# Kernel optimization log

Hardware: AMD Instinct MI355X
Metric: run time of the kernel (lower is better)

The kernel has to match this reference:

```python
import jax, jax.numpy as jnp
import numpy as np

THETA = 1.0
V_TH = 1.0       # spikingjelly IFNode default v_threshold
SG_ALPHA = 4.0   # spikingjelly surrogate.Sigmoid default alpha


@jax.custom_vjp
def heaviside(x):
    # spike = 1 if membrane - threshold >= 0
    return (x >= 0).astype(x.dtype)

def _heaviside_fwd(x):
    return (x >= 0).astype(x.dtype), x

def _heaviside_bwd(x, g):
    s = jax.nn.sigmoid(SG_ALPHA * x)
    return (g * SG_ALPHA * s * (1.0 - s),)

heaviside.defvjp(_heaviside_fwd, _heaviside_bwd)


@jax.custom_vjp
def spike_aggregate(spike_out, z_total):
    return spike_out

def _sa_fwd(spike_out, z_total):
    return spike_out, z_total

def _sa_bwd(z_total, g):
    surrogate = (z_total > 0).astype(g.dtype) / THETA
    return (jnp.zeros_like(g), g * surrogate)

spike_aggregate.defvjp(_sa_fwd, _sa_bwd)


def setup_inputs() -> dict:
    key = jax.random.key(0)
    k_x, k_w1, k_b1, k_w2, k_b2 = jax.random.split(key, 5)
    B, D_in, H, D_out = 4096, 784, 800, 10
    x = jax.random.uniform(k_x, (B, D_in), dtype=jnp.float32)
    # nn.Linear-style init: U(-1/sqrt(fan_in), 1/sqrt(fan_in))
    s1 = 1.0 / np.sqrt(D_in)
    s2 = 1.0 / np.sqrt(H)
    W1 = jax.random.uniform(k_w1, (H, D_in), jnp.float32, -s1, s1)
    b1 = jax.random.uniform(k_b1, (H,), jnp.float32, -s1, s1)
    W2 = jax.random.uniform(k_w2, (D_out, H), jnp.float32, -s2, s2)
    b2 = jax.random.uniform(k_b2, (D_out,), jnp.float32, -s2, s2)
    return {"x": x, "W1": W1, "b1": b1, "W2": W2, "b2": b2, "T_sim": 32}


def reference(x, W1, b1, W2, b2, T_sim):
    B = x.shape[0]
    x = x.reshape(B, -1)
    # fixed Bernoulli rate encoding (rand_like(x) < x)
    u = jax.random.uniform(jax.random.key(42), x.shape, dtype=x.dtype)
    x_fixed = (u < x).astype(x.dtype)
    # fc1 input is the same every timestep -> compute once
    cur1 = x_fixed @ W1.T + b1                     # [B, 800]

    def step(carry, _):
        v1, v2, count, z_total = carry
        h1 = v1 + cur1
        spk1 = heaviside(h1 - V_TH)
        v1 = h1 * (1.0 - jax.lax.stop_gradient(spk1))  # hard reset to 0, detach_reset
        cur2 = spk1 @ W2.T + b2                    # [B, 10]
        z_total = z_total + cur2
        h2 = v2 + cur2
        spk2 = heaviside(h2 - V_TH)
        v2 = h2 * (1.0 - jax.lax.stop_gradient(spk2))
        count = count + spk2
        return (v1, v2, count, z_total), None

    H, D_out = W1.shape[0], W2.shape[0]
    init = (jnp.zeros((B, H), x.dtype), jnp.zeros((B, D_out), x.dtype),
            jnp.zeros((B, D_out), x.dtype), jnp.zeros((B, D_out), x.dtype))
    (v1, v2, count, z_total), _ = jax.lax.scan(step, init, None, length=T_sim)
    return spike_aggregate(count, z_total)
```

## Files before the change

### kernel.cpp

```cpp
#include <hip/hip_runtime.h>
#include <stdint.h>

#define B_ROWS 4096
#define D_IN   784
#define H_DIM  800
#define D_OUT  10
#define T_SIM  32
#define N_ELEM (B_ROWS * D_IN)
#define CAP    448
#define R_PER  2

__device__ __forceinline__ void threefry2x32(uint32_t k0, uint32_t k1,
                                             uint32_t& x0, uint32_t& x1) {
  uint32_t ks0 = k0, ks1 = k1, ks2 = k0 ^ k1 ^ 0x1BD11BDAu;
  x0 += ks0; x1 += ks1;
#define TF_RND(r) { x0 += x1; x1 = (x1 << (r)) | (x1 >> (32 - (r))); x1 ^= x0; }
  TF_RND(13) TF_RND(15) TF_RND(26) TF_RND(6)
  x0 += ks1; x1 += ks2 + 1u;
  TF_RND(17) TF_RND(29) TF_RND(16) TF_RND(24)
  x0 += ks2; x1 += ks0 + 2u;
  TF_RND(13) TF_RND(15) TF_RND(26) TF_RND(6)
  x0 += ks0; x1 += ks1 + 3u;
  TF_RND(17) TF_RND(29) TF_RND(16) TF_RND(24)
  x0 += ks1; x1 += ks2 + 4u;
  TF_RND(13) TF_RND(15) TF_RND(26) TF_RND(6)
  x0 += ks2; x1 += ks0 + 5u;
#undef TF_RND
}

__global__ __launch_bounds__(256) void gen_xfixed(const float* __restrict__ x,
                                                  float* __restrict__ xf) {
  int i = blockIdx.x * blockDim.x + threadIdx.x;
  if (i >= N_ELEM) return;
  uint32_t c0 = 0u, c1 = (uint32_t)i;
  threefry2x32(0u, 42u, c0, c1);
  uint32_t bits = c0 ^ c1;
  float u = __uint_as_float((bits >> 9) | 0x3F800000u) - 1.0f;
  xf[i] = (u < x[i]) ? 1.0f : 0.0f;
}

#define BM 128
#define BN 64
#define BK 16

__global__ __launch_bounds__(256) void gemm_periods(const float* __restrict__ xf,
                                                    const float* __restrict__ W1,
                                                    const float* __restrict__ b1,
                                                    uint8_t* __restrict__ pb) {
  __shared__ __align__(16) float As[BK][BM + 4];
  __shared__ __align__(16) float Bs[BK][BN + 4];
  const int m0 = blockIdx.y * BM;
  const int n0 = blockIdx.x * BN;
  const int t  = threadIdx.x;
  const int tx = t & 15, ty = t >> 4;
  const int ar = t >> 1;
  const int ak = (t & 1) * 8;
  const int br = t >> 2;
  const int bk = (t & 3) * 4;
  const int hB = n0 + br;
  const bool bOK = (hB < H_DIM);
  const float* aptr = xf + (m0 + ar) * D_IN + ak;
  const float* bptr = W1 + (bOK ? hB : 0) * D_IN + bk;

  float4 a0 = *(const float4*)(aptr);
  float4 a1 = *(const float4*)(aptr + 4);
  float4 b0 = *(const float4*)(bptr);
  if (!bOK) { b0.x = b0.y = b0.z = b0.w = 0.0f; }

  float acc[8][4] = {};
  for (int kt = 0; kt < D_IN; kt += BK) {
    As[ak + 0][ar] = a0.x; As[ak + 1][ar] = a0.y;
    As[ak + 2][ar] = a0.z; As[ak + 3][ar] = a0.w;
    As[ak + 4][ar] = a1.x; As[ak + 5][ar] = a1.y;
    As[ak + 6][ar] = a1.z; As[ak + 7][ar] = a1.w;
    Bs[bk + 0][br] = b0.x; Bs[bk + 1][br] = b0.y;
    Bs[bk + 2][br] = b0.z; Bs[bk + 3][br] = b0.w;
    __syncthreads();
    if (kt + BK < D_IN) {
      a0 = *(const float4*)(aptr + kt + BK);
      a1 = *(const float4*)(aptr + kt + BK + 4);
      b0 = *(const float4*)(bptr + kt + BK);
      if (!bOK) { b0.x = b0.y = b0.z = b0.w = 0.0f; }
    }
#pragma unroll
    for (int kk = 0; kk < BK; kk++) {
      float4 av0 = *(const float4*)&As[kk][ty * 8];
      float4 av1 = *(const float4*)&As[kk][ty * 8 + 4];
      float4 bv  = *(const float4*)&Bs[kk][tx * 4];
      float a[8] = {av0.x, av0.y, av0.z, av0.w, av1.x, av1.y, av1.z, av1.w};
      float b[4] = {bv.x, bv.y, bv.z, bv.w};
#pragma unroll
      for (int mi = 0; mi < 8; mi++)
#pragma unroll
        for (int ni = 0; ni < 4; ni++)
          acc[mi][ni] = __builtin_fmaf(a[mi], b[ni], acc[mi][ni]);
    }
    __syncthreads();
  }
  const int hOut = n0 + tx * 4;
  if (hOut < H_DIM) {
    float4 bb = *(const float4*)&b1[hOut];
#pragma unroll
    for (int mi = 0; mi < 8; mi++) {
      int m = m0 + ty * 8 + mi;
      float c4[4];
      c4[0] = acc[mi][0] + bb.x;
      c4[1] = acc[mi][1] + bb.y;
      c4[2] = acc[mi][2] + bb.z;
      c4[3] = acc[mi][3] + bb.w;
      uint32_t packed = 0;
#pragma unroll
      for (int ni = 0; ni < 4; ni++) {
        float c = c4[ni];
        float v = 0.0f;
        int p = 0;
#pragma unroll 1
        for (int s = 1; s <= T_SIM; s++) {
          float h1 = v + c;
          if (h1 >= 1.0f) { p = s; break; }
          v = h1;
        }
        packed |= (uint32_t)p << (8 * ni);
      }
      *(uint32_t*)&pb[(size_t)m * H_DIM + hOut] = packed;
    }
  }
}

__global__ __launch_bounds__(320) void snn_scan(const uint8_t* __restrict__ pb,
                                                const float* __restrict__ W2,
                                                const float* __restrict__ b2,
                                                float* __restrict__ out) {
  __shared__ __align__(16) float W2T[H_DIM * D_OUT];
  __shared__ uint16_t ha16[R_PER][CAP];
  __shared__ uint32_t mks[R_PER][CAP];
  __shared__ int      lenL[R_PER];
  __shared__ uint32_t mask_tbl[T_SIM + 1];
  __shared__ float    c2s[R_PER][T_SIM][D_OUT];
  __shared__ float    b2f[D_OUT];
  const int tid  = threadIdx.x;
  const int row0 = blockIdx.x * R_PER;

  if (tid < D_OUT) b2f[tid] = b2[tid];
  if (tid <= T_SIM) {
    uint32_t mk = 0;
    if (tid > 0) for (int s = tid; s <= T_SIM; s += tid) mk |= 1u << (s - 1);
    mask_tbl[tid] = mk;
  }
  __syncthreads();

  if (tid < 128) {
    const int r = tid >> 6, ln = tid & 63;
    const uint64_t lmask = (1ull << ln) - 1ull;
    uint8_t pv[13];
#pragma unroll
    for (int ch = 0; ch < 13; ch++) {
      int h = ch * 64 + ln;
      pv[ch] = (h < H_DIM) ? pb[(size_t)(row0 + r) * H_DIM + h] : (uint8_t)0;
    }
    int off = 0;
#pragma unroll
    for (int ch = 0; ch < 13; ch++) {
      int h = ch * 64 + ln;
      int p = pv[ch];
      bool g = (p != 0);
      uint64_t bal = __ballot(g);
      int pos = off + __popcll(bal & lmask);
      if (g && pos < CAP) {
        ha16[r][pos] = (uint16_t)(h * 40);
        mks[r][pos]  = mask_tbl[p];
      }
      off += __popcll(bal);
    }
    if (ln == 0) lenL[r] = off;
  } else {
    for (int e = tid - 128; e < H_DIM * D_OUT; e += 192) {
      int o = e / H_DIM, h = e - o * H_DIM;
      W2T[h * D_OUT + o] = W2[e];
    }
  }
  __syncthreads();

  const int L0 = min(lenL[0], CAP), L1 = min(lenL[1], CAP);
  for (int e = tid; e < R_PER * CAP; e += 320) {
    int r = e / CAP, i = e - r * CAP;
    if (i >= (r ? L1 : L0)) { mks[r][i] = 0u; ha16[r][i] = 0; }
  }
  __syncthreads();

  {
    const int t = tid & 31, r = (tid >> 5) & 1, j = tid >> 6;
    float s0 = 0.0f, s1 = 0.0f;
    if (lenL[0] <= CAP && lenL[1] <= CAP) {
      const int Lmax = max(L0, L1);
      const uint16_t* hp = ha16[r];
      const uint32_t* mp = mks[r];
      const float*    wbase = W2T + 2 * j;
#pragma unroll 8
      for (int i = 0; i < Lmax; i++) {
        uint32_t ha = hp[i];
        uint32_t mk = mp[i];
        float2 w = *(const float2*)((const char*)wbase + ha);
        bool g = (mk >> t) & 1u;
        s0 += g ? w.x : 0.0f;
        s1 += g ? w.y : 0.0f;
      }
    } else {
      const uint8_t* prow = pb + (size_t)(row0 + r) * H_DIM;
      for (int h = 0; h < H_DIM; h++) {
        uint32_t mk = mask_tbl[prow[h]];
        float2 w = *(const float2*)&W2T[h * D_OUT + 2 * j];
        bool g = (mk >> t) & 1u;
        s0 += g ? w.x : 0.0f;
        s1 += g ? w.y : 0.0f;
      }
    }
    c2s[r][t][2 * j]     = s0;
    c2s[r][t][2 * j + 1] = s1;
  }
  __syncthreads();

  if (tid < R_PER * D_OUT) {
    const int r = tid / D_OUT, o = tid % D_OUT;
    const float bb = b2f[o];
    float v = 0.0f; int cnt = 0;
#pragma unroll
    for (int t = 0; t < T_SIM; t++) {
      float cur2 = c2s[r][t][o] + bb;
      float h2 = v + cur2;
      bool spk = (h2 >= 1.0f);
      cnt += spk ? 1 : 0;
      v = spk ? 0.0f : h2;
    }
    out[(size_t)(row0 + r) * D_OUT + o] = (float)cnt;
  }
}

extern "C" void kernel_launch(void* const* d_in, const int* in_sizes, int n_in,
                              void* d_out, int out_size, void* d_ws, size_t ws_size,
                              hipStream_t stream) {
  const float* x  = (const float*)d_in[0];
  const float* W1 = (const float*)d_in[1];
  const float* b1 = (const float*)d_in[2];
  const float* W2 = (const float*)d_in[3];
  const float* b2 = (const float*)d_in[4];
  float* outp = (float*)d_out;

  float*   xf = (float*)d_ws;
  uint8_t* pbuf = (uint8_t*)(xf + N_ELEM);

  gen_xfixed<<<N_ELEM / 256, 256, 0, stream>>>(x, xf);

  dim3 g1((H_DIM + BN - 1) / BN, B_ROWS / BM);
  gemm_periods<<<g1, 256, 0, stream>>>(xf, W1, b1, pbuf);

  snn_scan<<<B_ROWS / R_PER, 320, 0, stream>>>(pbuf, W2, b2, outp);
}
```

Before: 296.8 us.

## Gather W2 columns per active neuron into staged smem and widen scan block

```diff
diff --git a/kernel.cpp b/kernel.cpp
--- a/kernel.cpp
+++ b/kernel.cpp
@@ -7,8 +7,7 @@
 #define D_OUT  10
 #define T_SIM  32
 #define N_ELEM (B_ROWS * D_IN)
-#define CAP    448
-#define R_PER  2
+#define CAP    512
 
 __device__ __forceinline__ void threefry2x32(uint32_t k0, uint32_t k1,
                                              uint32_t& x0, uint32_t& x1) {
@@ -103,11 +102,8 @@
 #pragma unroll
     for (int mi = 0; mi < 8; mi++) {
       int m = m0 + ty * 8 + mi;
-      float c4[4];
-      c4[0] = acc[mi][0] + bb.x;
-      c4[1] = acc[mi][1] + bb.y;
-      c4[2] = acc[mi][2] + bb.z;
-      c4[3] = acc[mi][3] + bb.w;
+      float c4[4] = {acc[mi][0] + bb.x, acc[mi][1] + bb.y,
+                     acc[mi][2] + bb.z, acc[mi][3] + bb.w};
       uint32_t packed = 0;
 #pragma unroll
       for (int ni = 0; ni < 4; ni++) {
@@ -127,105 +123,122 @@
   }
 }
 
-__global__ __launch_bounds__(320) void snn_scan(const uint8_t* __restrict__ pb,
+__global__ __launch_bounds__(640) void snn_scan(const uint8_t* __restrict__ pb,
                                                 const float* __restrict__ W2,
                                                 const float* __restrict__ b2,
                                                 float* __restrict__ out) {
-  __shared__ __align__(16) float W2T[H_DIM * D_OUT];
-  __shared__ uint16_t ha16[R_PER][CAP];
-  __shared__ uint32_t mks[R_PER][CAP];
-  __shared__ int      lenL[R_PER];
-  __shared__ uint32_t mask_tbl[T_SIM + 1];
-  __shared__ float    c2s[R_PER][T_SIM][D_OUT];
+  __shared__ __align__(8) uint32_t mkS[2][CAP];
+  __shared__ uint16_t hidxS[2][CAP];
+  __shared__ __align__(16) float wst[2 * 5 * (CAP / 2) * 4];
+  __shared__ int      lenS[2];
+  __shared__ uint32_t mtbl[T_SIM + 1];
+  __shared__ float    c2s[2][T_SIM][D_OUT];
   __shared__ float    b2f[D_OUT];
   const int tid  = threadIdx.x;
-  const int row0 = blockIdx.x * R_PER;
-
-  if (tid < D_OUT) b2f[tid] = b2[tid];
+  const int row0 = blockIdx.x * 2;
+
   if (tid <= T_SIM) {
     uint32_t mk = 0;
-    if (tid > 0) for (int s = tid; s <= T_SIM; s += tid) mk |= 1u << (s - 1);
-    mask_tbl[tid] = mk;
-  }
+    if (tid) for (int s = tid; s <= T_SIM; s += tid) mk |= 1u << (s - 1);
+    mtbl[tid] = mk;
+  }
+  if (tid < D_OUT) b2f[tid] = b2[tid];
   __syncthreads();
 
   if (tid < 128) {
     const int r = tid >> 6, ln = tid & 63;
-    const uint64_t lmask = (1ull << ln) - 1ull;
+    const uint64_t lm = (1ull << ln) - 1ull;
+    const uint8_t* prow = pb + (size_t)(row0 + r) * H_DIM;
     uint8_t pv[13];
 #pragma unroll
-    for (int ch = 0; ch < 13; ch++) {
+    for (int ch = 0; ch < 13; ++ch) {
       int h = ch * 64 + ln;
-      pv[ch] = (h < H_DIM) ? pb[(size_t)(row0 + r) * H_DIM + h] : (uint8_t)0;
+      pv[ch] = (h < H_DIM) ? prow[h] : (uint8_t)0;
     }
     int off = 0;
 #pragma unroll
-    for (int ch = 0; ch < 13; ch++) {
-      int h = ch * 64 + ln;
-      int p = pv[ch];
-      bool g = (p != 0);
+    for (int ch = 0; ch < 13; ++ch) {
+      bool g = (pv[ch] != 0);
       uint64_t bal = __ballot(g);
-      int pos = off + __popcll(bal & lmask);
+      int pos = off + __popcll(bal & lm);
       if (g && pos < CAP) {
-        ha16[r][pos] = (uint16_t)(h * 40);
-        mks[r][pos]  = mask_tbl[p];
+        hidxS[r][pos] = (uint16_t)(ch * 64 + ln);
+        mkS[r][pos]   = mtbl[pv[ch]];
       }
       off += __popcll(bal);
     }
-    if (ln == 0) lenL[r] = off;
-  } else {
-    for (int e = tid - 128; e < H_DIM * D_OUT; e += 192) {
-      int o = e / H_DIM, h = e - o * H_DIM;
-      W2T[h * D_OUT + o] = W2[e];
-    }
-  }
-  __syncthreads();
-
-  const int L0 = min(lenL[0], CAP), L1 = min(lenL[1], CAP);
-  for (int e = tid; e < R_PER * CAP; e += 320) {
-    int r = e / CAP, i = e - r * CAP;
-    if (i >= (r ? L1 : L0)) { mks[r][i] = 0u; ha16[r][i] = 0; }
+    if (ln == 0) lenS[r] = off;
+  }
+  __syncthreads();
+
+  const int L0 = min(lenS[0], CAP), L1 = min(lenS[1], CAP);
+  const bool ovf = (lenS[0] > CAP) || (lenS[1] > CAP);
+  const int Lpad = (max(L0, L1) + 63) & ~63;
+
+  for (int e = tid; e < 2 * CAP; e += 640) {
+    int r = e >= CAP ? 1 : 0, i = e - r * CAP;
+    if (i >= (r ? L1 : L0)) mkS[r][i] = 0u;
   }
   __syncthreads();
 
   {
-    const int t = tid & 31, r = (tid >> 5) & 1, j = tid >> 6;
-    float s0 = 0.0f, s1 = 0.0f;
-    if (lenL[0] <= CAP && lenL[1] <= CAP) {
-      const int Lmax = max(L0, L1);
-      const uint16_t* hp = ha16[r];
-      const uint32_t* mp = mks[r];
-      const float*    wbase = W2T + 2 * j;
-#pragma unroll 8
-      for (int i = 0; i < Lmax; i++) {
-        uint32_t ha = hp[i];
-        uint32_t mk = mp[i];
-        float2 w = *(const float2*)((const char*)wbase + ha);
-        bool g = (mk >> t) & 1u;
-        s0 += g ? w.x : 0.0f;
-        s1 += g ? w.y : 0.0f;
+    const int npairs = Lpad >> 1;
+    for (int e = tid; e < 10 * npairs * 2; e += 640) {
+      int tmpe = e;
+      int hi = tmpe & 1; tmpe >>= 1;
+      int i2 = tmpe % npairs; tmpe /= npairs;
+      int j = tmpe % 5;  int r = tmpe / 5;
+      const int o = 2 * j + hi;
+      const int Lr = r ? L1 : L0;
+      float2 w;
+      int i0 = 2 * i2;
+      w.x = (i0     < Lr) ? W2[o * H_DIM + hidxS[r][i0]]     : 0.0f;
+      w.y = (i0 + 1 < Lr) ? W2[o * H_DIM + hidxS[r][i0 + 1]] : 0.0f;
+      *(float2*)&wst[((r * 5 + j) * (CAP / 2) + i2) * 4 + hi * 2] = w;
+    }
+  }
+  __syncthreads();
+
+  {
+    const int wv = tid >> 6;
+    const int r = wv & 1, j = wv >> 1;
+    const int lane = tid & 63;
+    const int t = lane & 31;
+    const int hi = lane >> 5;
+    float s = 0.0f;
+    if (!ovf) {
+      const uint32_t* mbase = mkS[r];
+      const float* wbase = &wst[(r * 5 + j) * (CAP / 2) * 4 + hi * 2];
+      const int npairs = Lpad >> 1;
+#pragma unroll 4
+      for (int i2 = 0; i2 < npairs; ++i2) {
+        uint2 mk2 = *(const uint2*)&mbase[2 * i2];
+        float2 w2 = *(const float2*)(wbase + i2 * 4);
+        float g0 = (float)((mk2.x >> t) & 1u);
+        s = __builtin_fmaf(g0, w2.x, s);
+        float g1 = (float)((mk2.y >> t) & 1u);
+        s = __builtin_fmaf(g1, w2.y, s);
       }
     } else {
       const uint8_t* prow = pb + (size_t)(row0 + r) * H_DIM;
-      for (int h = 0; h < H_DIM; h++) {
-        uint32_t mk = mask_tbl[prow[h]];
-        float2 w = *(const float2*)&W2T[h * D_OUT + 2 * j];
-        bool g = (mk >> t) & 1u;
-        s0 += g ? w.x : 0.0f;
-        s1 += g ? w.y : 0.0f;
-      }
-    }
-    c2s[r][t][2 * j]     = s0;
-    c2s[r][t][2 * j + 1] = s1;
-  }
-  __syncthreads();
-
-  if (tid < R_PER * D_OUT) {
+      const int o = 2 * j + hi;
+      const uint32_t vbit = 1u << t;
+      for (int h = 0; h < H_DIM; ++h) {
+        uint32_t mk = mtbl[prow[h]];
+        float w = W2[o * H_DIM + h];
+        s += (mk & vbit) ? w : 0.0f;
+      }
+    }
+    c2s[r][t][2 * j + hi] = s;
+  }
+  __syncthreads();
+
+  if (tid < 2 * D_OUT) {
     const int r = tid / D_OUT, o = tid % D_OUT;
     const float bb = b2f[o];
     float v = 0.0f; int cnt = 0;
 #pragma unroll
-    for (int t = 0; t < T_SIM; t++) {
+    for (int t = 0; t < T_SIM; ++t) {
       float cur2 = c2s[r][t][o] + bb;
       float h2 = v + cur2;
       bool spk = (h2 >= 1.0f);
@@ -254,5 +267,5 @@
   dim3 g1((H_DIM + BN - 1) / BN, B_ROWS / BM);
   gemm_periods<<<g1, 256, 0, stream>>>(xf, W1, b1, pbuf);
 
-  snn_scan<<<B_ROWS / R_PER, 320, 0, stream>>>(pbuf, W2, b2, outp);
-}
+  snn_scan<<<B_ROWS / 2, 640, 0, stream>>>(pbuf, W2, b2, outp);
+}
```

Measured after the change: 315.7 us. +6.4%, slower.
